# Kernel optimization log

Measured on AMD Instinct MI355X. Metric: run time of the kernel, lower is better.

Reference implementation:

```python
import jax, jax.numpy as jnp
import numpy as np

N_NODES = 100000
N_EDGES = 1600000
H_FEATS = 128
OUT_CLASSES = 6


def setup_inputs() -> dict:
    key = jax.random.key(0)
    ks = jax.random.split(key, 9)
    h = jax.random.normal(ks[0], (N_NODES, H_FEATS), dtype=jnp.float32)
    src = jax.random.randint(ks[1], (N_EDGES,), 0, N_NODES)
    dst = jax.random.randint(ks[2], (N_EDGES,), 0, N_NODES)
    # torch nn.Linear convention: y = x @ W.T + b, W shape [out, in]
    W1 = jax.random.normal(ks[3], (64, 2 * H_FEATS), dtype=jnp.float32) * 0.05
    b1 = jax.random.normal(ks[4], (64,), dtype=jnp.float32) * 0.05
    W2 = jax.random.normal(ks[5], (32, 64), dtype=jnp.float32) * 0.05
    b2 = jax.random.normal(ks[6], (32,), dtype=jnp.float32) * 0.05
    W3 = jax.random.normal(ks[7], (OUT_CLASSES, 32), dtype=jnp.float32) * 0.05
    b3 = jax.random.normal(ks[8], (OUT_CLASSES,), dtype=jnp.float32) * 0.05
    return {"h": h, "src": src, "dst": dst, "W1": W1, "b1": b1,
            "W2": W2, "b2": b2, "W3": W3, "b3": b3}


def reference(h, src, dst, W1, b1, W2, b2, W3, b3):
    # Per-edge gather of src/dst node features, concat -> [E, 2*H]
    x = jnp.concatenate([h[src], h[dst]], axis=1)
    x = jax.nn.relu(x @ W1.T + b1)   # [E, 64]
    x = jax.nn.relu(x @ W2.T + b2)   # [E, 32]
    return x @ W3.T + b3             # [E, output_class]
```

## Files before the change

kernel.cpp:

```cpp
#include <hip/hip_runtime.h>
#include <hip/hip_bf16.h>
#include <stdint.h>


#define H 128

typedef short bf16x8 __attribute__((ext_vector_type(8)));
typedef float f32x4  __attribute__((ext_vector_type(4)));

__device__ __forceinline__ uint16_t f2bf(float f) {
    uint32_t u = __float_as_uint(f);
    return (uint16_t)((u + 0x7fffu + ((u >> 16) & 1u)) >> 16);
}
__device__ __forceinline__ uint32_t pk_bf16(float lo, float hi) {
    __hip_bfloat162 v = __float22bfloat162_rn(float2{lo, hi});
    return *reinterpret_cast<uint32_t*>(&v);
}
__device__ __forceinline__ uint32_t bfadd2_relu(uint32_t a, uint32_t b) {
    __hip_bfloat162 x = *reinterpret_cast<__hip_bfloat162*>(&a);
    __hip_bfloat162 y = *reinterpret_cast<__hip_bfloat162*>(&b);
    __hip_bfloat162 s = __hadd2(x, y);
    uint32_t zu = 0u;
    __hip_bfloat162 zero = *reinterpret_cast<__hip_bfloat162*>(&zu);
    __hip_bfloat162 r = __hmax2(s, zero);
    return *reinterpret_cast<uint32_t*>(&r);
}

__global__ void prep_weights(const float* __restrict__ W1,
                             const float* __restrict__ W2,
                             const float* __restrict__ W3,
                             uint16_t* __restrict__ Bfrag,
                             uint16_t* __restrict__ EFrag)
{
    int t = blockIdx.x * blockDim.x + threadIdx.x;
    int stride = gridDim.x * blockDim.x;
    for (int i = t; i < 4 * 8 * 64 * 8; i += stride) {
        int j    = i & 7;
        int lane = (i >> 3) & 63;
        int nt   = (i >> 9) & 7;
        int kt   = (i >> 12);
        int k = kt * 32 + (lane >> 4) * 8 + j;
        int n = nt * 16 + (lane & 15);
        float v = (n < 64) ? W1[n * 256 + k] : W1[(n - 64) * 256 + 128 + k];
        Bfrag[i] = f2bf(v);
    }
    for (int i = t; i < 5 * 64 * 8; i += stride) {
        int j    = i & 7;
        int lane = (i >> 3) & 63;
        int f    = i >> 9;
        uint16_t v;
        if (f < 4) {
            int kt = f >> 1, nt = f & 1;
            int k = kt * 32 + (lane >> 4) * 8 + j;
            int n = nt * 16 + (lane & 15);
            v = f2bf(W2[n * 64 + k]);
        } else {
            int k = (lane >> 4) * 8 + j;
            int n = lane & 15;
            v = (n < 6) ? f2bf(W3[n * 32 + k]) : (uint16_t)0;
        }
        EFrag[i] = v;
    }
}

__global__ void __launch_bounds__(256) node_gemm(
    const float* __restrict__ h,
    const uint16_t* __restrict__ Bfrag,
    const float* __restrict__ b1,
    uint16_t* __restrict__ pre, int N)
{
    const int wave = threadIdx.x >> 6;
    const int lane = threadIdx.x & 63;
    const int n0 = (blockIdx.x * 4 + wave) * 32;
    if (n0 >= N) return;

    const int m    = lane & 15;
    const int quad = lane >> 4;

    bf16x8 afr[2][4];
#pragma unroll
    for (int mt = 0; mt < 2; mt++) {
        int arow = n0 + mt * 16 + m; if (arow >= N) arow = N - 1;
        const float* hrow = h + (size_t)arow * H + quad * 8;
#pragma unroll
        for (int kt = 0; kt < 4; kt++) {
            float4 lo = *(const float4*)(hrow + kt * 32);
            float4 hi = *(const float4*)(hrow + kt * 32 + 4);
            union { bf16x8 v; uint32_t u[4]; } A;
            A.u[0] = pk_bf16(lo.x, lo.y); A.u[1] = pk_bf16(lo.z, lo.w);
            A.u[2] = pk_bf16(hi.x, hi.y); A.u[3] = pk_bf16(hi.z, hi.w);
            afr[mt][kt] = A.v;
        }
    }

#pragma unroll
    for (int nt = 0; nt < 8; nt++) {
        const int n = nt * 16 + m;
        f32x4 acc0 = {0.f, 0.f, 0.f, 0.f};
        f32x4 acc1 = {0.f, 0.f, 0.f, 0.f};
#pragma unroll
        for (int kt = 0; kt < 4; kt++) {
            bf16x8 bfr = *(const bf16x8*)(Bfrag + ((size_t)(kt * 8 + nt) * 64 + lane) * 8);
            acc0 = __builtin_amdgcn_mfma_f32_16x16x32_bf16(afr[0][kt], bfr, acc0, 0, 0, 0);
            acc1 = __builtin_amdgcn_mfma_f32_16x16x32_bf16(afr[1][kt], bfr, acc1, 0, 0, 0);
        }
        const float bv = (n < 64) ? b1[n] : 0.f;
#pragma unroll
        for (int r = 0; r < 4; r++) {
            const int node0 = n0 + quad * 4 + r;
            if (node0 < N) pre[(size_t)node0 * H + n] = f2bf(acc0[r] + bv);
            const int node1 = n0 + 16 + quad * 4 + r;
            if (node1 < N) pre[(size_t)node1 * H + n] = f2bf(acc1[r] + bv);
        }
    }
}

__global__ void __launch_bounds__(256) edge_mlp(
    const uint16_t* __restrict__ pre,
    const int* __restrict__ src, const int* __restrict__ dst,
    const uint16_t* __restrict__ EFrag,
    const float* __restrict__ b2, const float* __restrict__ b3,
    float* __restrict__ out, long E)
{
    __shared__ uint16_t zbuf[4][64 * 40];

    const int wave = threadIdx.x >> 6;
    const int lane = threadIdx.x & 63;
    const int m15  = lane & 15;
    const int quad = lane >> 4;
    uint16_t* zw = &zbuf[wave][0];

    bf16x8 bL2[4], bL3;
#pragma unroll
    for (int f = 0; f < 4; f++) bL2[f] = *(const bf16x8*)(EFrag + (f * 64 + lane) * 8);
    bL3 = *(const bf16x8*)(EFrag + (4 * 64 + lane) * 8);
    const float vb2a = b2[m15];
    const float vb2b = b2[16 + m15];
    const float vb3  = (m15 < 6) ? b3[m15] : 0.f;

    const long e0 = (long)(blockIdx.x * 4 + wave) * 64;
    if (e0 >= E) return;

    const char* preb = (const char*)pre;
    uint32_t oa0, oa1, oa2, oa3, ob0, ob1, ob2, ob3;
    {
        long ea = e0 + m15;
        long eb = (ea + 16 < E) ? ea + 16 : E - 1;
        long ec = (ea + 32 < E) ? ea + 32 : E - 1;
        long ed = (ea + 48 < E) ? ea + 48 : E - 1;
        if (ea >= E) ea = E - 1;
        oa0 = (uint32_t)src[ea] * 256u + (uint32_t)quad * 16u;
        ob0 = (uint32_t)dst[ea] * 256u + 128u + (uint32_t)quad * 16u;
        oa1 = (uint32_t)src[eb] * 256u + (uint32_t)quad * 16u;
        ob1 = (uint32_t)dst[eb] * 256u + 128u + (uint32_t)quad * 16u;
        oa2 = (uint32_t)src[ec] * 256u + (uint32_t)quad * 16u;
        ob2 = (uint32_t)dst[ec] * 256u + 128u + (uint32_t)quad * 16u;
        oa3 = (uint32_t)src[ed] * 256u + (uint32_t)quad * 16u;
        ob3 = (uint32_t)dst[ed] * 256u + 128u + (uint32_t)quad * 16u;
    }
    uint4 a00 = *(const uint4*)(preb + oa0);
    uint4 a01 = *(const uint4*)(preb + oa0 + 64);
    uint4 b00 = *(const uint4*)(preb + ob0);
    uint4 b01 = *(const uint4*)(preb + ob0 + 64);
    uint4 a10 = *(const uint4*)(preb + oa1);
    uint4 a11 = *(const uint4*)(preb + oa1 + 64);
    uint4 b10 = *(const uint4*)(preb + ob1);
    uint4 b11 = *(const uint4*)(preb + ob1 + 64);
    uint4 a20 = *(const uint4*)(preb + oa2);
    uint4 a21 = *(const uint4*)(preb + oa2 + 64);
    uint4 b20 = *(const uint4*)(preb + ob2);
    uint4 b21 = *(const uint4*)(preb + ob2 + 64);
    uint4 a30 = *(const uint4*)(preb + oa3);
    uint4 a31 = *(const uint4*)(preb + oa3 + 64);
    uint4 b30 = *(const uint4*)(preb + ob3);
    uint4 b31 = *(const uint4*)(preb + ob3 + 64);

#define DO_SUBTILE(ST, UA0, UB0, UA1, UB1)                                        \
    {                                                                             \
        union { bf16x8 v; uint32_t u[4]; } A0, A1;                                \
        A0.u[0] = bfadd2_relu(UA0.x, UB0.x);                                      \
        A0.u[1] = bfadd2_relu(UA0.y, UB0.y);                                      \
        A0.u[2] = bfadd2_relu(UA0.z, UB0.z);                                      \
        A0.u[3] = bfadd2_relu(UA0.w, UB0.w);                                      \
        A1.u[0] = bfadd2_relu(UA1.x, UB1.x);                                      \
        A1.u[1] = bfadd2_relu(UA1.y, UB1.y);                                      \
        A1.u[2] = bfadd2_relu(UA1.z, UB1.z);                                      \
        A1.u[3] = bfadd2_relu(UA1.w, UB1.w);                                      \
        _Pragma("unroll")                                                         \
        for (int nt = 0; nt < 2; nt++) {                                          \
            f32x4 acc = {0.f, 0.f, 0.f, 0.f};                                     \
            acc = __builtin_amdgcn_mfma_f32_16x16x32_bf16(A0.v, bL2[nt], acc, 0, 0, 0); \
            acc = __builtin_amdgcn_mfma_f32_16x16x32_bf16(A1.v, bL2[2 + nt], acc, 0, 0, 0); \
            const float vb2 = nt ? vb2b : vb2a;                                   \
            _Pragma("unroll")                                                     \
            for (int r = 0; r < 4; r++) {                                         \
                float z = fmaxf(acc[r] + vb2, 0.f);                               \
                zw[((ST) * 16 + quad * 4 + r) * 40 + nt * 16 + m15] = f2bf(z);    \
            }                                                                     \
        }                                                                         \
    }

    DO_SUBTILE(0, a00, b00, a01, b01)
    DO_SUBTILE(1, a10, b10, a11, b11)
    DO_SUBTILE(2, a20, b20, a21, b21)
    DO_SUBTILE(3, a30, b30, a31, b31)
#undef DO_SUBTILE

#pragma unroll
    for (int st = 0; st < 4; st++) {
        bf16x8 a3 = *(const bf16x8*)(zw + (st * 16 + m15) * 40 + quad * 8);
        f32x4 o = {0.f, 0.f, 0.f, 0.f};
        o = __builtin_amdgcn_mfma_f32_16x16x32_bf16(a3, bL3, o, 0, 0, 0);
        if (m15 < 6) {
#pragma unroll
            for (int r = 0; r < 4; r++) {
                long e = e0 + st * 16 + quad * 4 + r;
                if (e < E) out[e * 6 + m15] = o[r] + vb3;
            }
        }
    }
}

extern "C" void kernel_launch(void* const* d_in, const int* in_sizes, int n_in,
                              void* d_out, int out_size, void* d_ws, size_t ws_size,
                              hipStream_t stream) {
    const float* h   = (const float*)d_in[0];
    const int*   src = (const int*)d_in[1];
    const int*   dst = (const int*)d_in[2];
    const float* W1  = (const float*)d_in[3];
    const float* b1  = (const float*)d_in[4];
    const float* W2  = (const float*)d_in[5];
    const float* b2  = (const float*)d_in[6];
    const float* W3  = (const float*)d_in[7];
    const float* b3  = (const float*)d_in[8];

    const int  N = in_sizes[0] / H;
    const long E = in_sizes[1];

    char* ws = (char*)d_ws;
    uint16_t* Bfrag = (uint16_t*)ws;
    uint16_t* EFrag = (uint16_t*)(ws + 64 * 1024);
    uint16_t* pre   = (uint16_t*)(ws + 128 * 1024);

    prep_weights<<<64, 256, 0, stream>>>(W1, W2, W3, Bfrag, EFrag);
    node_gemm<<<(N + 127) / 128, 256, 0, stream>>>(h, Bfrag, b1, pre, N);
    const int eblocks = (int)((E + 255) / 256);
    edge_mlp<<<eblocks, 256, 0, stream>>>(pre, src, dst, EFrag, b2, b3,
                                          (float*)d_out, E);
}
```

Measured before the change: 183.0 us.

## Compute layer-2 transposed to keep activations in registers, dropping the LDS round-trip

Layer 2 is reformulated as W2 × Yᵀ, with W2 rows permuted in the fragment packing, so the MFMA output lands in each lane already laid out as the A operand of the layer-3 MFMA. This removes the shared-memory staging buffer, the scattered 16-bit LDS stores and the reload between layers 2 and 3. It also lowers LDS use, which may help occupancy. The cost is a more intricate row permutation in the weight prep and per-lane bias vectors, where an indexing mistake would break correctness.

```diff
diff --git a/kernel.cpp b/kernel.cpp
--- a/kernel.cpp
+++ b/kernel.cpp
@@ -50,10 +50,11 @@
         int f    = i >> 9;
         uint16_t v;
         if (f < 4) {
-            int kt = f >> 1, nt = f & 1;
-            int k = kt * 32 + (lane >> 4) * 8 + j;
-            int n = nt * 16 + (lane & 15);
-            v = f2bf(W2[n * 64 + k]);
+            int nt = f >> 1, kt = f & 1;
+            int m  = lane & 15;
+            int row = (m >> 2) * 8 + (m & 3) + 4 * nt;
+            int col = kt * 32 + (lane >> 4) * 8 + j;
+            v = f2bf(W2[row * 64 + col]);
         } else {
             int k = (lane >> 4) * 8 + j;
             int n = lane & 15;
@@ -122,23 +123,24 @@
     const float* __restrict__ b2, const float* __restrict__ b3,
     float* __restrict__ out, long E)
 {
-    __shared__ uint16_t zbuf[4][64 * 40];
-
-    const int wave = threadIdx.x >> 6;
     const int lane = threadIdx.x & 63;
     const int m15  = lane & 15;
     const int quad = lane >> 4;
-    uint16_t* zw = &zbuf[wave][0];
-
-    bf16x8 bL2[4], bL3;
-#pragma unroll
-    for (int f = 0; f < 4; f++) bL2[f] = *(const bf16x8*)(EFrag + (f * 64 + lane) * 8);
+
+    bf16x8 w2a[4], bL3;
+#pragma unroll
+    for (int f = 0; f < 4; f++) w2a[f] = *(const bf16x8*)(EFrag + (f * 64 + lane) * 8);
     bL3 = *(const bf16x8*)(EFrag + (4 * 64 + lane) * 8);
-    const float vb2a = b2[m15];
-    const float vb2b = b2[16 + m15];
-    const float vb3  = (m15 < 6) ? b3[m15] : 0.f;
-
-    const long e0 = (long)(blockIdx.x * 4 + wave) * 64;
+    float vb2j[8];
+    {
+        float4 t0 = *(const float4*)(b2 + quad * 8);
+        float4 t1 = *(const float4*)(b2 + quad * 8 + 4);
+        vb2j[0] = t0.x; vb2j[1] = t0.y; vb2j[2] = t0.z; vb2j[3] = t0.w;
+        vb2j[4] = t1.x; vb2j[5] = t1.y; vb2j[6] = t1.z; vb2j[7] = t1.w;
+    }
+    const float vb3 = (m15 < 6) ? b3[m15] : 0.f;
+
+    const long e0 = (long)(blockIdx.x * 4 + (threadIdx.x >> 6)) * 64;
     if (e0 >= E) return;
 
     const char* preb = (const char*)pre;
@@ -177,25 +179,33 @@
 
 #define DO_SUBTILE(ST, UA0, UB0, UA1, UB1)                                        \
     {                                                                             \
-        union { bf16x8 v; uint32_t u[4]; } A0, A1;                                \
-        A0.u[0] = bfadd2_relu(UA0.x, UB0.x);                                      \
-        A0.u[1] = bfadd2_relu(UA0.y, UB0.y);                                      \
-        A0.u[2] = bfadd2_relu(UA0.z, UB0.z);                                      \
-        A0.u[3] = bfadd2_relu(UA0.w, UB0.w);                                      \
-        A1.u[0] = bfadd2_relu(UA1.x, UB1.x);                                      \
-        A1.u[1] = bfadd2_relu(UA1.y, UB1.y);                                      \
-        A1.u[2] = bfadd2_relu(UA1.z, UB1.z);                                      \
-        A1.u[3] = bfadd2_relu(UA1.w, UB1.w);                                      \
-        _Pragma("unroll")                                                         \
-        for (int nt = 0; nt < 2; nt++) {                                          \
-            f32x4 acc = {0.f, 0.f, 0.f, 0.f};                                     \
-            acc = __builtin_amdgcn_mfma_f32_16x16x32_bf16(A0.v, bL2[nt], acc, 0, 0, 0); \
-            acc = __builtin_amdgcn_mfma_f32_16x16x32_bf16(A1.v, bL2[2 + nt], acc, 0, 0, 0); \
-            const float vb2 = nt ? vb2b : vb2a;                                   \
+        union { bf16x8 v; uint32_t u[4]; } Y0, Y1;                                \
+        Y0.u[0] = bfadd2_relu(UA0.x, UB0.x);                                      \
+        Y0.u[1] = bfadd2_relu(UA0.y, UB0.y);                                      \
+        Y0.u[2] = bfadd2_relu(UA0.z, UB0.z);                                      \
+        Y0.u[3] = bfadd2_relu(UA0.w, UB0.w);                                      \
+        Y1.u[0] = bfadd2_relu(UA1.x, UB1.x);                                      \
+        Y1.u[1] = bfadd2_relu(UA1.y, UB1.y);                                      \
+        Y1.u[2] = bfadd2_relu(UA1.z, UB1.z);                                      \
+        Y1.u[3] = bfadd2_relu(UA1.w, UB1.w);                                      \
+        f32x4 z0 = {0.f, 0.f, 0.f, 0.f};             \
+        f32x4 z1 = {0.f, 0.f, 0.f, 0.f};             \
+        z0 = __builtin_amdgcn_mfma_f32_16x16x32_bf16(w2a[0], Y0.v, z0, 0, 0, 0);  \
+        z0 = __builtin_amdgcn_mfma_f32_16x16x32_bf16(w2a[1], Y1.v, z0, 0, 0, 0);  \
+        z1 = __builtin_amdgcn_mfma_f32_16x16x32_bf16(w2a[2], Y0.v, z1, 0, 0, 0);  \
+        z1 = __builtin_amdgcn_mfma_f32_16x16x32_bf16(w2a[3], Y1.v, z1, 0, 0, 0);  \
+        union { bf16x8 v; uint32_t u[4]; } A3;                                    \
+        A3.u[0] = pk_bf16(fmaxf(z0[0] + vb2j[0], 0.f), fmaxf(z0[1] + vb2j[1], 0.f)); \
+        A3.u[1] = pk_bf16(fmaxf(z0[2] + vb2j[2], 0.f), fmaxf(z0[3] + vb2j[3], 0.f)); \
+        A3.u[2] = pk_bf16(fmaxf(z1[0] + vb2j[4], 0.f), fmaxf(z1[1] + vb2j[5], 0.f)); \
+        A3.u[3] = pk_bf16(fmaxf(z1[2] + vb2j[6], 0.f), fmaxf(z1[3] + vb2j[7], 0.f)); \
+        f32x4 o = {0.f, 0.f, 0.f, 0.f};                                           \
+        o = __builtin_amdgcn_mfma_f32_16x16x32_bf16(A3.v, bL3, o, 0, 0, 0);       \
+        if (m15 < 6) {                                                            \
             _Pragma("unroll")                                                     \
             for (int r = 0; r < 4; r++) {                                         \
-                float z = fmaxf(acc[r] + vb2, 0.f);                               \
-                zw[((ST) * 16 + quad * 4 + r) * 40 + nt * 16 + m15] = f2bf(z);    \
+                long e = e0 + (ST) * 16 + quad * 4 + r;                           \
+                if (e < E) out[(size_t)e * 6 + m15] = o[r] + vb3;                 \
             }                                                                     \
         }                                                                         \
     }
@@ -205,20 +215,6 @@
     DO_SUBTILE(2, a20, b20, a21, b21)
     DO_SUBTILE(3, a30, b30, a31, b31)
 #undef DO_SUBTILE
-
-#pragma unroll
-    for (int st = 0; st < 4; st++) {
-        bf16x8 a3 = *(const bf16x8*)(zw + (st * 16 + m15) * 40 + quad * 8);
-        f32x4 o = {0.f, 0.f, 0.f, 0.f};
-        o = __builtin_amdgcn_mfma_f32_16x16x32_bf16(a3, bL3, o, 0, 0, 0);
-        if (m15 < 6) {
-#pragma unroll
-            for (int r = 0; r < 4; r++) {
-                long e = e0 + st * 16 + quad * 4 + r;
-                if (e < E) out[e * 6 + m15] = o[r] + vb3;
-            }
-        }
-    }
 }
 
 extern "C" void kernel_launch(void* const* d_in, const int* in_sizes, int n_in,
```

Result: no change. 184.9 us (+1.0%).
